# Kernel tuning notes

Hardware: AMD Instinct MI355X
Metric: run time of the kernel (lower is better)

The kernel has to match this reference:

```python
import math
import jax, jax.numpy as jnp
import numpy as np

B, S, DIM = 1, 2048, 2880
N_HEADS, N_KV, HD = 64, 8, 64
ROPE_FACTOR = 32.0
THETA = 150000.0
NEG_INF = -1e30


def setup_inputs() -> dict:
    key = jax.random.key(0)
    ks = jax.random.split(key, 12)
    std = 0.02
    x = jax.random.normal(ks[0], (B, S, DIM), jnp.float32)
    # rope cache: (S, 2*HD) = [cos | sin], rotate_half convention (angles duplicated)
    inv_freq = 1.0 / (THETA ** (np.arange(0, HD, 2, dtype=np.float32) / HD))
    angles = np.arange(S, dtype=np.float32)[:, None] * inv_freq[None, :]   # (S, HD/2)
    emb = np.concatenate([angles, angles], axis=-1)                        # (S, HD)
    rope_cache = jnp.asarray(np.concatenate([np.cos(emb), np.sin(emb)], axis=-1))  # (S, 2*HD)
    wq_w = jax.random.normal(ks[1], (N_HEADS * HD, DIM), jnp.float32) * std
    wq_b = jax.random.normal(ks[2], (N_HEADS * HD,), jnp.float32) * std
    wk_w = jax.random.normal(ks[3], (N_KV * HD, DIM), jnp.float32) * std
    wk_b = jax.random.normal(ks[4], (N_KV * HD,), jnp.float32) * std
    wv_w = jax.random.normal(ks[5], (N_KV * HD, DIM), jnp.float32) * std
    wv_b = jax.random.normal(ks[6], (N_KV * HD,), jnp.float32) * std
    wo_w = jax.random.normal(ks[7], (DIM, N_HEADS * HD), jnp.float32) * std
    wo_b = jax.random.normal(ks[8], (DIM,), jnp.float32) * std
    sinks = jax.random.normal(ks[9], (N_HEADS,), jnp.float32) * std
    return {"x": x, "rope_cache": rope_cache, "wq_w": wq_w, "wq_b": wq_b,
            "wk_w": wk_w, "wk_b": wk_b, "wv_w": wv_w, "wv_b": wv_b,
            "wo_w": wo_w, "wo_b": wo_b, "sinks": sinks, "sliding_window": 128}


def _rotate_half(t):
    t1, t2 = t[..., : HD // 2], t[..., HD // 2 :]
    return jnp.concatenate([-t2, t1], axis=-1)


def reference(x, rope_cache, wq_w, wq_b, wk_w, wk_b, wv_w, wv_b, wo_w, wo_b, sinks, sliding_window):
    bsz, seqlen, _ = x.shape
    mscale = 0.1 * math.log(ROPE_FACTOR) + 1.0
    scale = mscale / math.sqrt(HD)

    q = (x @ wq_w.T + wq_b).reshape(bsz, seqlen, N_HEADS, HD)
    k = (x @ wk_w.T + wk_b).reshape(bsz, seqlen, N_KV, HD)
    v = (x @ wv_w.T + wv_b).reshape(bsz, seqlen, N_KV, HD)

    cos = rope_cache[:seqlen, :HD][None, :, None, :]   # (1,S,1,HD)
    sin = rope_cache[:seqlen, HD:][None, :, None, :]
    q = q * cos + _rotate_half(q) * sin
    k = k * cos + _rotate_half(k) * sin

    q = q.transpose(0, 2, 1, 3)                        # (B,H,S,hd)
    n_rep = N_HEADS // N_KV
    k = jnp.repeat(k.transpose(0, 2, 1, 3), n_rep, axis=1)  # GQA expand
    v = jnp.repeat(v.transpose(0, 2, 1, 3), n_rep, axis=1)

    scores = jnp.einsum("bhqd,bhkd->bhqk", q, k) * scale
    i = jnp.arange(seqlen)[:, None]
    j = jnp.arange(seqlen)[None, :]
    mask = (j <= i) & ((i - j) < sliding_window)       # causal + sliding window
    scores = jnp.where(mask[None, None], scores, NEG_INF)

    lse = jax.nn.logsumexp(scores, axis=-1)            # (B,H,S)
    attn = jax.nn.softmax(scores, axis=-1)
    out = jnp.einsum("bhqk,bhkd->bhqd", attn, v)

    sink_scale = jax.nn.sigmoid(lse - sinks[None, :, None])[..., None]
    out = out * sink_scale

    out = out.transpose(0, 2, 1, 3).reshape(bsz, seqlen, N_HEADS * HD)
    return out @ wo_w.T + wo_b
```

## Files before the change

kernel.cpp:

```cpp
#include <hip/hip_runtime.h>
#include <hip/hip_bf16.h>
#include <math.h>
#include <stdint.h>


typedef __bf16 bf16x8 __attribute__((ext_vector_type(8)));
typedef float  f32x4  __attribute__((ext_vector_type(4)));
typedef uint32_t u32x4 __attribute__((ext_vector_type(4)));

#define MFMA_BF16(a,b,c) __builtin_amdgcn_mfma_f32_16x16x32_bf16((a),(b),(c),0,0,0)

#define XB   0L
#define WQB  5898240L
#define WKB  17694720L
#define WVB  19169280L
#define WOB  20643840L
#define QB   32440320L
#define KB   40828928L
#define VB   41877504L

__device__ __forceinline__ void gld_lds16(const void* g, void* l) {
    __builtin_amdgcn_global_load_lds(
        (__attribute__((address_space(1))) void*)(g),
        (__attribute__((address_space(3))) void*)(l), 16, 0, 0);
}

__device__ __forceinline__ bf16x8 ld8f(const float* p) {
    f32x4 a = *(const f32x4*)p;
    f32x4 b = *(const f32x4*)(p + 4);
    bf16x8 r;
#pragma unroll
    for (int t = 0; t < 4; t++) { r[t] = (__bf16)a[t]; r[t + 4] = (__bf16)b[t]; }
    return r;
}

__device__ __forceinline__ uint32_t pack2(float a, float b) {
    __bf16 x = (__bf16)a, y = (__bf16)b;
    return (uint32_t)__builtin_bit_cast(unsigned short, x)
         | ((uint32_t)__builtin_bit_cast(unsigned short, y) << 16);
}

__global__ __launch_bounds__(256) void convert_kernel(
    const float* __restrict__ x,  const float* __restrict__ wq,
    const float* __restrict__ wk, const float* __restrict__ wv,
    const float* __restrict__ wo, __bf16* __restrict__ dst)
{
    long e = ((long)blockIdx.x * 256 + threadIdx.x) * 8;
    const float* src; long off;
    if      (e <  WQB) { src = x;  off = e; }
    else if (e <  WKB) { src = wq; off = e - WQB; }
    else if (e <  WVB) { src = wk; off = e - WKB; }
    else if (e <  WOB) { src = wv; off = e - WVB; }
    else               { src = wo; off = e - WOB; }
    *(bf16x8*)(dst + e) = ld8f(src + off);
}

__device__ __forceinline__ void gemm_block64(
    const __bf16* __restrict__ A, const __bf16* __restrict__ W,
    const float* __restrict__ bias, __bf16* __restrict__ C,
    int N, int Ks, int kBeg, int kEnd, int m0, int n0,
    __bf16* As, __bf16* Bs)
{
    const int tid  = threadIdx.x;
    const int lane = tid & 63;
    const int wv   = tid >> 6;
    const int wm   = (wv >> 1) * 64;
    const int wn   = (wv & 1) * 64;
    const int quad = lane >> 4;
    const int c    = lane & 15;

    const int srow = tid >> 2;
    const int scol = (tid & 3) * 8;

    int br0 = n0 + srow;      if (br0 > N - 1) br0 = N - 1;
    int br1 = n0 + 64 + srow; if (br1 > N - 1) br1 = N - 1;
    const __bf16* pa0 = A + (size_t)(m0 + srow) * Ks + scol;
    const __bf16* pa1 = A + (size_t)(m0 + 64 + srow) * Ks + scol;
    const __bf16* pb0 = W + (size_t)br0 * Ks + scol;
    const __bf16* pb1 = W + (size_t)br1 * Ks + scol;

    f32x4 acc[4][4];
#pragma unroll
    for (int i = 0; i < 4; i++)
#pragma unroll
        for (int j = 0; j < 4; j++) acc[i][j] = (f32x4){0.f, 0.f, 0.f, 0.f};

    for (int kk = kBeg; kk < kEnd; kk += 64) {
        gld_lds16(pa0 + kk,      As + tid * 8);
        gld_lds16(pa1 + kk,      As + 2048 + tid * 8);
        gld_lds16(pa0 + kk + 32, As + 4096 + tid * 8);
        gld_lds16(pa1 + kk + 32, As + 6144 + tid * 8);
        gld_lds16(pb0 + kk,      Bs + tid * 8);
        gld_lds16(pb1 + kk,      Bs + 2048 + tid * 8);
        gld_lds16(pb0 + kk + 32, Bs + 4096 + tid * 8);
        gld_lds16(pb1 + kk + 32, Bs + 6144 + tid * 8);
        __syncthreads();
        for (int kt = 0; kt < 2; kt++) {
            bf16x8 af[4], bfv[4];
#pragma unroll
            for (int i = 0; i < 4; i++)
                af[i] = *(const bf16x8*)&As[kt * 4096 + (wm + i * 16 + c) * 32 + quad * 8];
#pragma unroll
            for (int j = 0; j < 4; j++)
                bfv[j] = *(const bf16x8*)&Bs[kt * 4096 + (wn + j * 16 + c) * 32 + quad * 8];
#pragma unroll
            for (int i = 0; i < 4; i++)
#pragma unroll
                for (int j = 0; j < 4; j++)
                    acc[i][j] = MFMA_BF16(af[i], bfv[j], acc[i][j]);
        }
        __syncthreads();
    }

#pragma unroll
    for (int j = 0; j < 4; j++) {
        int col = n0 + wn + j * 16 + c;
        if (col >= N) continue;
        float bv = bias ? bias[col] : 0.0f;
#pragma unroll
        for (int i = 0; i < 4; i++) {
            int row = m0 + wm + i * 16 + quad * 4;
#pragma unroll
            for (int r = 0; r < 4; r++)
                C[(size_t)(row + r) * N + col] = (__bf16)(acc[i][j][r] + bv);
        }
    }
}

__global__ __launch_bounds__(256, 3) void qkv_kernel(
    const __bf16* __restrict__ x,
    const __bf16* __restrict__ wq, const float* __restrict__ bq,
    const __bf16* __restrict__ wk, const float* __restrict__ bk,
    const __bf16* __restrict__ wv, const float* __restrict__ bv,
    __bf16* __restrict__ qo, __bf16* __restrict__ ko, __bf16* __restrict__ vo)
{
    __shared__ __align__(16) __bf16 As[8192], Bs[8192];
    const int orig = blockIdx.y * 16 + blockIdx.x;
    const int wg   = (orig & 7) * 80 + (orig >> 3);
    const int bx   = wg & 15;
    const int by   = wg >> 4;
    const __bf16 *W; const float* bias; __bf16* C; int N, n0;
    if (by < 32)      { W = wq; bias = bq; C = qo; N = 4096; n0 = by * 128; }
    else if (by < 36) { W = wk; bias = bk; C = ko; N = 512;  n0 = (by - 32) * 128; }
    else              { W = wv; bias = bv; C = vo; N = 512;  n0 = (by - 36) * 128; }
    gemm_block64(x, W, bias, C, N, 2880, 0, 2880, bx * 128, n0, As, Bs);
}

__global__ __launch_bounds__(256, 3) void oproj_kernel(
    const __bf16* __restrict__ a, const __bf16* __restrict__ w,
    __bf16* __restrict__ p0, __bf16* __restrict__ p1)
{
    __shared__ __align__(16) __bf16 As[8192], Bs[8192];
    const int z = blockIdx.z;
    __bf16* C = z ? p1 : p0;
    const int orig = blockIdx.y * 16 + blockIdx.x;
    const int wg   = (orig & 7) * 46 + (orig >> 3);
    const int bx   = wg & 15;
    const int by   = wg >> 4;
    gemm_block64(a, w, nullptr, C, 2880, 4096, z * 2048, (z + 1) * 2048,
                 bx * 128, by * 128, As, Bs);
}

__global__ __launch_bounds__(256) void reduce_kernel(
    const __bf16* __restrict__ p0, const __bf16* __restrict__ p1,
    const float* __restrict__ bo, float* __restrict__ out)
{
    long e = ((long)blockIdx.x * 256 + threadIdx.x) * 8;
    int col = (int)(e % 2880L);
    bf16x8 a = *(const bf16x8*)(p0 + e);
    bf16x8 b = *(const bf16x8*)(p1 + e);
    f32x4 o0, o1;
#pragma unroll
    for (int t = 0; t < 4; t++) {
        o0[t] = (float)a[t]     + (float)b[t]     + bo[col + t];
        o1[t] = (float)a[4 + t] + (float)b[4 + t] + bo[col + 4 + t];
    }
    *(f32x4*)(out + e)     = o0;
    *(f32x4*)(out + e + 4) = o1;
}

template<int F>
__device__ __forceinline__ void attn_f_step(
    const __bf16* __restrict__ Ks, const __bf16* __restrict__ Vt,
    __bf16* __restrict__ q, bf16x8 qf0, bf16x8 qf1,
    int i0, int h, int k0, float sk,
    int c, int quad, int laneA, int laneB, bool hiSel, int db)
{
    f32x4 acc9[9];
#pragma unroll
    for (int jj = 0; jj < 9; jj++) acc9[jj] = (f32x4){0.f, 0.f, 0.f, 0.f};
    __builtin_amdgcn_s_setprio(1);
#pragma unroll
    for (int jj = 0; jj < 9; jj++) {
        const int j = F + jj;
        bf16x8 kf0 = *(const bf16x8*)&Ks[(j * 16 + c) * 72 + quad * 8];
        bf16x8 kf1 = *(const bf16x8*)&Ks[(j * 16 + c) * 72 + 32 + quad * 8];
        acc9[jj] = MFMA_BF16(kf0, qf0, acc9[jj]);
        acc9[jj] = MFMA_BF16(kf1, qf1, acc9[jj]);
    }
    __builtin_amdgcn_s_setprio(0);

    const int jgb = k0 + F * 16 + quad * 4;
    float rmax = -3.0e4f;
#pragma unroll
    for (int jj = 0; jj < 9; jj++)
#pragma unroll
        for (int r = 0; r < 4; r++) {
            int d  = db  - jj * 16 - r;
            int jg = jgb + jj * 16 + r;
            bool ok = ((unsigned)d < 128u) && (jg >= 0);
            float vv = ok ? acc9[jj][r] : -3.0e4f;
            acc9[jj][r] = vv;
            rmax = fmaxf(rmax, vv);
        }
    rmax = fmaxf(rmax, __shfl_xor(rmax, 16));
    rmax = fmaxf(rmax, __shfl_xor(rmax, 32));

    float rs = 0.f;
#pragma unroll
    for (int jj = 0; jj < 9; jj++)
#pragma unroll
        for (int r = 0; r < 4; r++) {
            float e = __expf(acc9[jj][r] - rmax);
            acc9[jj][r] = e;
            rs += e;
        }
    rs += __shfl_xor(rs, 16);
    rs += __shfl_xor(rs, 32);

    float s   = fmaxf(rs, 1e-20f);
    float lse = rmax + __logf(s);
    float fac = 1.f / ((1.f + __expf(sk - lse)) * s);

    uint32_t pk[20];
#pragma unroll
    for (int t = 0; t < 20; t++) pk[t] = 0;
#pragma unroll
    for (int jj = 0; jj < 9; jj++) {
        const int li = (F & 1) ? (2 * jj + 2) : (2 * jj);
        pk[li]     = pack2(acc9[jj][0] * fac, acc9[jj][1] * fac);
        pk[li + 1] = pack2(acc9[jj][2] * fac, acc9[jj][3] * fac);
    }

    f32x4 acc2[4];
#pragma unroll
    for (int jd = 0; jd < 4; jd++) acc2[jd] = (f32x4){0.f, 0.f, 0.f, 0.f};
#pragma unroll
    for (int kk = 0; kk < 5; kk++) {
        const int kt = (F >> 1) + kk;
        uint32_t l0  = (uint32_t)__shfl((int)pk[4 * kk],     laneA);
        uint32_t h0  = (uint32_t)__shfl((int)pk[4 * kk + 1], laneA);
        uint32_t l0b = (uint32_t)__shfl((int)pk[4 * kk],     laneB);
        uint32_t h0b = (uint32_t)__shfl((int)pk[4 * kk + 1], laneB);
        uint32_t l1  = (uint32_t)__shfl((int)pk[4 * kk + 2], laneA);
        uint32_t h1  = (uint32_t)__shfl((int)pk[4 * kk + 3], laneA);
        uint32_t l1b = (uint32_t)__shfl((int)pk[4 * kk + 2], laneB);
        uint32_t h1b = (uint32_t)__shfl((int)pk[4 * kk + 3], laneB);
        u32x4 wvv = { hiSel ? l1  : l0,  hiSel ? h1  : h0,
                      hiSel ? l1b : l0b, hiSel ? h1b : h0b };
        bf16x8 pa = __builtin_bit_cast(bf16x8, wvv);
        __builtin_amdgcn_s_setprio(1);
#pragma unroll
        for (int jd = 0; jd < 4; jd++) {
            bf16x8 bv = *(const bf16x8*)&Vt[(jd * 16 + c) * 200 + kt * 32 + quad * 8];
            acc2[jd] = MFMA_BF16(pa, bv, acc2[jd]);
        }
        __builtin_amdgcn_s_setprio(0);
    }

#pragma unroll
    for (int jd = 0; jd < 4; jd++)
#pragma unroll
        for (int r = 0; r < 4; r++)
            q[(size_t)(i0 + F * 16 + quad * 4 + r) * 4096 + h * 64 + jd * 16 + c]
                = (__bf16)acc2[jd][r];
}

__global__ __launch_bounds__(512) void attn_kernel(
    __bf16* __restrict__ q, const __bf16* __restrict__ k,
    const __bf16* __restrict__ v, const float* __restrict__ sinks,
    const float* __restrict__ rope)
{
    __shared__ __align__(16) __bf16 Ks[192 * 72];
    __shared__ __align__(16) __bf16 Vt[64 * 200];

    const int tid = threadIdx.x, lane = tid & 63, w = tid >> 6;
    const int quad = lane >> 4, c = lane & 15;
    const int i0  = blockIdx.x * 64;
    const int kvh = blockIdx.y;
    const int h   = kvh * 8 + w;
    const int k0  = i0 - 128;
    const float scale = 0.16832169878499658f;

#pragma unroll
    for (int it = 0; it < 2; it++) {
        int unit = it * 512 + tid;
        if (unit < 768) {
            int krow = unit >> 2;
            int kdg  = (unit & 3) * 8;
            int j = k0 + krow; if (j < 0) j = 0;
            const __bf16* gp = k + (size_t)j * 512 + kvh * 64 + kdg;
            bf16x8 x1 = *(const bf16x8*)(gp);
            bf16x8 x2 = *(const bf16x8*)(gp + 32);
            const float* rc = rope + (size_t)j * 128 + kdg;
            bf16x8 o1, o2;
#pragma unroll
            for (int t = 0; t < 8; t++) {
                float cc = rc[t], si = rc[64 + t];
                float a = (float)x1[t], b = (float)x2[t];
                o1[t] = (__bf16)(a * cc - b * si);
                o2[t] = (__bf16)(b * cc + a * si);
            }
            *(bf16x8*)&Ks[krow * 72 + kdg]      = o1;
            *(bf16x8*)&Ks[krow * 72 + kdg + 32] = o2;
        }
    }

    {
        const int vrow = tid & 63;
        const int d0   = (tid >> 6) * 8;
#pragma unroll
        for (int it = 0; it < 3; it++) {
            int s = it * 64 + vrow;
            int j = k0 + s; if (j < 0) j = 0;
            bf16x8 t = *(const bf16x8*)(v + (size_t)j * 512 + kvh * 64 + d0);
#pragma unroll
            for (int u = 0; u < 8; u++) Vt[(d0 + u) * 200 + s] = t[u];
        }
    }

    bf16x8 qf[4][2];
#pragma unroll
    for (int f = 0; f < 4; f++) {
        const int row = i0 + f * 16 + c;
        const __bf16* gp = q + (size_t)row * 4096 + h * 64 + quad * 8;
        bf16x8 x1 = *(const bf16x8*)(gp);
        bf16x8 x2 = *(const bf16x8*)(gp + 32);
        const float* rc = rope + (size_t)row * 128 + quad * 8;
        bf16x8 o1, o2;
#pragma unroll
        for (int t = 0; t < 8; t++) {
            float cc = rc[t] * scale, si = rc[64 + t] * scale;
            float a = (float)x1[t], b = (float)x2[t];
            o1[t] = (__bf16)(a * cc - b * si);
            o2[t] = (__bf16)(b * cc + a * si);
        }
        qf[f][0] = o1; qf[f][1] = o2;
    }

    __syncthreads();

    const float sk   = sinks[h];
    const int laneA  = ((quad & 1) << 5) + c;
    const int laneB  = laneA + 16;
    const bool hiSel = (quad >> 1) != 0;
    const int db     = 128 + c - quad * 4;

    attn_f_step<0>(Ks, Vt, q, qf[0][0], qf[0][1], i0, h, k0, sk, c, quad, laneA, laneB, hiSel, db);
    attn_f_step<1>(Ks, Vt, q, qf[1][0], qf[1][1], i0, h, k0, sk, c, quad, laneA, laneB, hiSel, db);
    attn_f_step<2>(Ks, Vt, q, qf[2][0], qf[2][1], i0, h, k0, sk, c, quad, laneA, laneB, hiSel, db);
    attn_f_step<3>(Ks, Vt, q, qf[3][0], qf[3][1], i0, h, k0, sk, c, quad, laneA, laneB, hiSel, db);
}

extern "C" void kernel_launch(void* const* d_in, const int* in_sizes, int n_in,
                              void* d_out, int out_size, void* d_ws, size_t ws_size,
                              hipStream_t stream) {
    const float* x    = (const float*)d_in[0];
    const float* rope = (const float*)d_in[1];
    const float* wq   = (const float*)d_in[2];
    const float* bq   = (const float*)d_in[3];
    const float* wk   = (const float*)d_in[4];
    const float* bk   = (const float*)d_in[5];
    const float* wv   = (const float*)d_in[6];
    const float* bv   = (const float*)d_in[7];
    const float* wo   = (const float*)d_in[8];
    const float* bo   = (const float*)d_in[9];
    const float* sk   = (const float*)d_in[10];
    float* out = (float*)d_out;

    __bf16* wsb = (__bf16*)d_ws;
    __bf16* xb  = wsb + XB;
    __bf16* wqb = wsb + WQB;
    __bf16* wkb = wsb + WKB;
    __bf16* wvb = wsb + WVB;
    __bf16* wob = wsb + WOB;
    __bf16* qb  = wsb + QB;
    __bf16* kb  = wsb + KB;
    __bf16* vb  = wsb + VB;
    __bf16* po0 = wsb + 0L;
    __bf16* po1 = wsb + 5898240L;

    convert_kernel<<<15840, 256, 0, stream>>>(x, wq, wk, wv, wo, xb);
    qkv_kernel<<<dim3(16, 40), 256, 0, stream>>>(xb, wqb, bq, wkb, bk, wvb, bv,
                                                 qb, kb, vb);
    attn_kernel<<<dim3(32, 8), 512, 0, stream>>>(qb, kb, vb, sk, rope);
    oproj_kernel<<<dim3(16, 23, 2), 256, 0, stream>>>(qb, wob, po0, po1);
    reduce_kernel<<<2880, 256, 0, stream>>>(po0, po1, bo, out);
}
```

Baseline: 330.1 us.

## Double-buffer GEMMs with 256x256 tiles, 512 threads and XOR-swizzled LDS

Replaces the 128x128 single-buffered GEMM core with a 256x256 tile computed by 8 waves, each producing 128x64. LDS is double-buffered so global-to-LDS loads for step t+2 are issued while step t is computed, controlled by explicit vmcnt waits and barriers. The LDS layout uses an XOR swizzle to avoid bank conflicts. MFMA sections raise wave priority. Larger tiles cut global traffic per flop, but they give fewer workgroups (160 for QKV, 192 for the o-projection), which may underfill the 256 CUs, and they use much more LDS and registers per block.

```diff
diff --git a/kernel.cpp b/kernel.cpp
--- a/kernel.cpp
+++ b/kernel.cpp
@@ -55,7 +55,22 @@
     *(bf16x8*)(dst + e) = ld8f(src + off);
 }
 
-__device__ __forceinline__ void gemm_block64(
+__device__ __forceinline__ void stage256(
+    const __bf16* pa0, const __bf16* pb0, const __bf16* pb1,
+    const __bf16* pb2, const __bf16* pb3, size_t aStep, int kk,
+    __bf16* Asb, __bf16* Bsb, int tid)
+{
+    gld_lds16(pa0 + kk,             Asb + (tid        ) * 8);
+    gld_lds16(pa0 + aStep + kk,     Asb + (tid +  512 ) * 8);
+    gld_lds16(pa0 + 2 * aStep + kk, Asb + (tid + 1024 ) * 8);
+    gld_lds16(pa0 + 3 * aStep + kk, Asb + (tid + 1536 ) * 8);
+    gld_lds16(pb0 + kk,             Bsb + (tid        ) * 8);
+    gld_lds16(pb1 + kk,             Bsb + (tid +  512 ) * 8);
+    gld_lds16(pb2 + kk,             Bsb + (tid + 1024 ) * 8);
+    gld_lds16(pb3 + kk,             Bsb + (tid + 1536 ) * 8);
+}
+
+__device__ __forceinline__ void gemm256(
     const __bf16* __restrict__ A, const __bf16* __restrict__ W,
     const float* __restrict__ bias, __bf16* __restrict__ C,
     int N, int Ks, int kBeg, int kEnd, int m0, int n0,
@@ -64,62 +79,82 @@
     const int tid  = threadIdx.x;
     const int lane = tid & 63;
     const int wv   = tid >> 6;
-    const int wm   = (wv >> 1) * 64;
-    const int wn   = (wv & 1) * 64;
+    const int wr   = wv >> 2;
+    const int wc   = wv & 3;
     const int quad = lane >> 4;
     const int c    = lane & 15;
 
-    const int srow = tid >> 2;
-    const int scol = (tid & 3) * 8;
-
-    int br0 = n0 + srow;      if (br0 > N - 1) br0 = N - 1;
-    int br1 = n0 + 64 + srow; if (br1 > N - 1) br1 = N - 1;
-    const __bf16* pa0 = A + (size_t)(m0 + srow) * Ks + scol;
-    const __bf16* pa1 = A + (size_t)(m0 + 64 + srow) * Ks + scol;
-    const __bf16* pb0 = W + (size_t)br0 * Ks + scol;
-    const __bf16* pb1 = W + (size_t)br1 * Ks + scol;
-
-    f32x4 acc[4][4];
-#pragma unroll
-    for (int i = 0; i < 4; i++)
+    const int srow = tid >> 3;
+    const int scg2 = (tid & 7) ^ (srow & 7);
+
+    const __bf16* pa0 = A + (size_t)(m0 + srow) * Ks + scg2 * 8;
+    const size_t aStep = (size_t)64 * Ks;
+    const __bf16* pb[4];
+#pragma unroll
+    for (int i = 0; i < 4; i++) {
+        int br = n0 + srow + 64 * i; if (br > N - 1) br = N - 1;
+        pb[i] = W + (size_t)br * Ks + scg2 * 8;
+    }
+
+    const int NT = (kEnd - kBeg) >> 6;
+
+    f32x4 acc[8][4];
+#pragma unroll
+    for (int i = 0; i < 8; i++)
 #pragma unroll
         for (int j = 0; j < 4; j++) acc[i][j] = (f32x4){0.f, 0.f, 0.f, 0.f};
 
-    for (int kk = kBeg; kk < kEnd; kk += 64) {
-        gld_lds16(pa0 + kk,      As + tid * 8);
-        gld_lds16(pa1 + kk,      As + 2048 + tid * 8);
-        gld_lds16(pa0 + kk + 32, As + 4096 + tid * 8);
-        gld_lds16(pa1 + kk + 32, As + 6144 + tid * 8);
-        gld_lds16(pb0 + kk,      Bs + tid * 8);
-        gld_lds16(pb1 + kk,      Bs + 2048 + tid * 8);
-        gld_lds16(pb0 + kk + 32, Bs + 4096 + tid * 8);
-        gld_lds16(pb1 + kk + 32, Bs + 6144 + tid * 8);
-        __syncthreads();
+    stage256(pa0, pb[0], pb[1], pb[2], pb[3], aStep, kBeg,      As,         Bs,         tid);
+    stage256(pa0, pb[0], pb[1], pb[2], pb[3], aStep, kBeg + 64, As + 16384, Bs + 16384, tid);
+    asm volatile("s_waitcnt vmcnt(8)" ::: "memory");
+    __builtin_amdgcn_sched_barrier(0);
+    __builtin_amdgcn_s_barrier();
+
+    const int fxor = c & 7;
+
+    for (int t = 0; t < NT; ++t) {
+        __builtin_amdgcn_sched_barrier(0);
+        const __bf16* Ab = As + (t & 1) * 16384;
+        const __bf16* Bb = Bs + (t & 1) * 16384;
+#pragma unroll
         for (int kt = 0; kt < 2; kt++) {
-            bf16x8 af[4], bfv[4];
-#pragma unroll
-            for (int i = 0; i < 4; i++)
-                af[i] = *(const bf16x8*)&As[kt * 4096 + (wm + i * 16 + c) * 32 + quad * 8];
+            const int ko = ((kt * 4 + quad) ^ fxor) * 8;
+            bf16x8 af[8], bfv[4];
+#pragma unroll
+            for (int i = 0; i < 8; i++)
+                af[i] = *(const bf16x8*)&Ab[(wr * 128 + i * 16 + c) * 64 + ko];
 #pragma unroll
             for (int j = 0; j < 4; j++)
-                bfv[j] = *(const bf16x8*)&Bs[kt * 4096 + (wn + j * 16 + c) * 32 + quad * 8];
-#pragma unroll
-            for (int i = 0; i < 4; i++)
+                bfv[j] = *(const bf16x8*)&Bb[(wc * 64 + j * 16 + c) * 64 + ko];
+            __builtin_amdgcn_s_setprio(1);
+#pragma unroll
+            for (int i = 0; i < 8; i++)
 #pragma unroll
                 for (int j = 0; j < 4; j++)
                     acc[i][j] = MFMA_BF16(af[i], bfv[j], acc[i][j]);
-        }
-        __syncthreads();
+            __builtin_amdgcn_s_setprio(0);
+        }
+        __builtin_amdgcn_sched_barrier(0);
+        __builtin_amdgcn_s_barrier();
+        if (t + 2 < NT) {
+            stage256(pa0, pb[0], pb[1], pb[2], pb[3], aStep, kBeg + (t + 2) * 64,
+                     As + (t & 1) * 16384, Bs + (t & 1) * 16384, tid);
+            asm volatile("s_waitcnt vmcnt(8)" ::: "memory");
+        } else {
+            asm volatile("s_waitcnt vmcnt(0)" ::: "memory");
+        }
+        __builtin_amdgcn_sched_barrier(0);
+        __builtin_amdgcn_s_barrier();
     }
 
 #pragma unroll
     for (int j = 0; j < 4; j++) {
-        int col = n0 + wn + j * 16 + c;
+        int col = n0 + wc * 64 + j * 16 + c;
         if (col >= N) continue;
         float bv = bias ? bias[col] : 0.0f;
 #pragma unroll
-        for (int i = 0; i < 4; i++) {
-            int row = m0 + wm + i * 16 + quad * 4;
+        for (int i = 0; i < 8; i++) {
+            int row = m0 + wr * 128 + i * 16 + quad * 4;
 #pragma unroll
             for (int r = 0; r < 4; r++)
                 C[(size_t)(row + r) * N + col] = (__bf16)(acc[i][j][r] + bv);
@@ -127,38 +162,38 @@
     }
 }
 
-__global__ __launch_bounds__(256, 3) void qkv_kernel(
+__global__ __launch_bounds__(512, 2) void qkv_kernel(
     const __bf16* __restrict__ x,
     const __bf16* __restrict__ wq, const float* __restrict__ bq,
     const __bf16* __restrict__ wk, const float* __restrict__ bk,
     const __bf16* __restrict__ wv, const float* __restrict__ bv,
     __bf16* __restrict__ qo, __bf16* __restrict__ ko, __bf16* __restrict__ vo)
 {
-    __shared__ __align__(16) __bf16 As[8192], Bs[8192];
-    const int orig = blockIdx.y * 16 + blockIdx.x;
-    const int wg   = (orig & 7) * 80 + (orig >> 3);
-    const int bx   = wg & 15;
-    const int by   = wg >> 4;
+    __shared__ __align__(16) __bf16 As[2 * 16384], Bs[2 * 16384];
+    const int lin = blockIdx.y * 8 + blockIdx.x;
+    const int wg  = (lin & 7) * 20 + (lin >> 3);
+    const int m0  = (wg & 7) * 256;
+    const int by2 = wg >> 3;
     const __bf16 *W; const float* bias; __bf16* C; int N, n0;
-    if (by < 32)      { W = wq; bias = bq; C = qo; N = 4096; n0 = by * 128; }
-    else if (by < 36) { W = wk; bias = bk; C = ko; N = 512;  n0 = (by - 32) * 128; }
-    else              { W = wv; bias = bv; C = vo; N = 512;  n0 = (by - 36) * 128; }
-    gemm_block64(x, W, bias, C, N, 2880, 0, 2880, bx * 128, n0, As, Bs);
-}
-
-__global__ __launch_bounds__(256, 3) void oproj_kernel(
+    if (by2 < 16)      { W = wq; bias = bq; C = qo; N = 4096; n0 = by2 * 256; }
+    else if (by2 < 18) { W = wk; bias = bk; C = ko; N = 512;  n0 = (by2 - 16) * 256; }
+    else               { W = wv; bias = bv; C = vo; N = 512;  n0 = (by2 - 18) * 256; }
+    gemm256(x, W, bias, C, N, 2880, 0, 2880, m0, n0, As, Bs);
+}
+
+__global__ __launch_bounds__(512, 2) void oproj_kernel(
     const __bf16* __restrict__ a, const __bf16* __restrict__ w,
     __bf16* __restrict__ p0, __bf16* __restrict__ p1)
 {
-    __shared__ __align__(16) __bf16 As[8192], Bs[8192];
+    __shared__ __align__(16) __bf16 As[2 * 16384], Bs[2 * 16384];
     const int z = blockIdx.z;
     __bf16* C = z ? p1 : p0;
-    const int orig = blockIdx.y * 16 + blockIdx.x;
-    const int wg   = (orig & 7) * 46 + (orig >> 3);
-    const int bx   = wg & 15;
-    const int by   = wg >> 4;
-    gemm_block64(a, w, nullptr, C, 2880, 4096, z * 2048, (z + 1) * 2048,
-                 bx * 128, by * 128, As, Bs);
+    const int lin = blockIdx.y * 8 + blockIdx.x;
+    const int wg  = (lin & 7) * 12 + (lin >> 3);
+    const int m0  = (wg & 7) * 256;
+    const int by2 = wg >> 3;
+    gemm256(a, w, nullptr, C, 2880, 4096, z * 2048, (z + 1) * 2048,
+            m0, by2 * 256, As, Bs);
 }
 
 __global__ __launch_bounds__(256) void reduce_kernel(
@@ -391,9 +426,9 @@
     __bf16* po1 = wsb + 5898240L;
 
     convert_kernel<<<15840, 256, 0, stream>>>(x, wq, wk, wv, wo, xb);
-    qkv_kernel<<<dim3(16, 40), 256, 0, stream>>>(xb, wqb, bq, wkb, bk, wvb, bv,
-                                                 qb, kb, vb);
+    qkv_kernel<<<dim3(8, 20), 512, 0, stream>>>(xb, wqb, bq, wkb, bk, wvb, bv,
+                                                qb, kb, vb);
     attn_kernel<<<dim3(32, 8), 512, 0, stream>>>(qb, kb, vb, sk, rope);
-    oproj_kernel<<<dim3(16, 23, 2), 256, 0, stream>>>(qb, wob, po0, po1);
+    oproj_kernel<<<dim3(8, 12, 2), 512, 0, stream>>>(qb, wob, po0, po1);
     reduce_kernel<<<2880, 256, 0, stream>>>(po0, po1, bo, out);
 }
```

After: 363.2 us. +10.0%, slower.
